# Kernel optimization log

Measured on AMD Instinct MI355X. Metric: run time of the kernel, lower is better.

Reference implementation:

```python
import jax, jax.numpy as jnp
import numpy as np
from jax import lax

B, S, D = 16, 1024, 1024
PE = 20          # positioning_embedding (LSTM hidden)
NB = 3           # num_building_blocks
EPS = 1e-12      # F.normalize eps


def setup_inputs() -> dict:
    key = jax.random.key(0)
    ks = jax.random.split(key, 10)
    s = lambda *sh: 0.05
    inp = {
        "x": jax.random.normal(ks[0], (B, S, D), dtype=jnp.float32),
        # LSTM params (PyTorch layout: gates ordered i,f,g,o)
        "W_ih": jax.random.normal(ks[1], (4 * PE, D), dtype=jnp.float32) * 0.02,
        "W_hh": jax.random.normal(ks[2], (4 * PE, PE), dtype=jnp.float32) * 0.02,
        "b_ih": jax.random.normal(ks[3], (4 * PE,), dtype=jnp.float32) * 0.02,
        "b_hh": jax.random.normal(ks[4], (4 * PE,), dtype=jnp.float32) * 0.02,
        # mu_generator: Linear(PE -> NB)
        "W_mu": jax.random.normal(ks[5], (NB, PE), dtype=jnp.float32) * 0.1,
        "b_mu": jax.random.normal(ks[6], (NB,), dtype=jnp.float32) * 0.1,
        # sigma_generator: Linear(PE -> 1)
        "W_sig": jax.random.normal(ks[7], (1, PE), dtype=jnp.float32) * 0.1,
        "b_sig": jax.random.normal(ks[8], (1,), dtype=jnp.float32) * 0.1,
    }
    return inp


def _lstm(x, W_ih, W_hh, b_ih, b_hh):
    # x: [B, S, D] -> h: [B, S, PE]; single-layer batch_first LSTM, h0=c0=0
    b, _, _ = x.shape
    H = W_hh.shape[1]
    xg = jnp.einsum("bsd,gd->bsg", x, W_ih) + b_ih + b_hh  # [B,S,4H]

    def step(carry, xg_t):
        h, c = carry
        g = xg_t + h @ W_hh.T
        i, f, gg, o = jnp.split(g, 4, axis=-1)
        c = jax.nn.sigmoid(f) * c + jax.nn.sigmoid(i) * jnp.tanh(gg)
        h = jax.nn.sigmoid(o) * jnp.tanh(c)
        return (h, c), h

    init = (jnp.zeros((b, H), x.dtype), jnp.zeros((b, H), x.dtype))
    _, hs = lax.scan(step, init, xg.transpose(1, 0, 2))  # hs: [S,B,H]
    return hs.transpose(1, 0, 2)


def _forward(x, W_ih, W_hh, b_ih, b_hh, W_mu, b_mu, W_sig, b_sig):
    b, s, d = x.shape
    pw = _lstm(x, W_ih, W_hh, b_ih, b_hh)                       # [B,S,PE]
    mu_w = jax.nn.relu(jnp.einsum("bsp,np->bsn", pw, W_mu) + b_mu)   # [B,S,3]
    sigma = jax.nn.sigmoid(jnp.einsum("bsp,op->bso", pw, W_sig) + b_sig)[..., 0]  # [B,S]

    # sequential mu recurrence: mu_j = w0*prev_mu + w1*(1/S) + w2*(j+1)/S
    j_idx = jnp.arange(s, dtype=x.dtype)

    def mu_step(prev_mu, inputs):
        w_t, j = inputs  # w_t: [B,3]
        mu = w_t[:, 0] * prev_mu + w_t[:, 1] / s + w_t[:, 2] * (j + 1.0) / s
        return mu, mu

    _, mus = lax.scan(mu_step, jnp.zeros((b,), x.dtype),
                      (mu_w.transpose(1, 0, 2), j_idx))          # mus: [S,B]
    mu = mus.T                                                    # [B,S]

    # triangular relative positions: rel[j,i] = i/(j+1) for i<=j
    i_idx = jnp.arange(s, dtype=x.dtype)
    rel = i_idx[None, :] / (j_idx[:, None] + 1.0)                 # [S,S]
    mask = i_idx[None, :] <= j_idx[:, None]                       # lower-triangular

    w = jnp.exp(-((rel[None] - mu[:, :, None]) ** 2)
                / (2.0 * sigma[:, :, None] ** 2))                 # [B,S,S]
    w = jnp.where(mask[None], w, 0.0)
    # F.normalize over the position axis (L2)
    norm = jnp.sqrt(jnp.sum(w * w, axis=-1, keepdims=True))
    w = w / jnp.maximum(norm, EPS)

    context = jnp.einsum("bji,bid->bjd", w, x)                    # [B,S,D]
    return context


def reference(x, W_ih, W_hh, b_ih, b_hh, W_mu, b_mu, W_sig, b_sig):
    return _forward(x, W_ih, W_hh, b_ih, b_hh, W_mu, b_mu, W_sig, b_sig)
```

## Files before the change

### kernel.cpp

```cpp
#include <hip/hip_runtime.h>

#define DEVFN __device__ __forceinline__

static constexpr int cB  = 16;
static constexpr int cS  = 1024;
static constexpr int cD  = 1024;
static constexpr int cPE = 20;
static constexpr int cG  = 80;

typedef float  floatx2  __attribute__((ext_vector_type(2)));
typedef float  floatx4  __attribute__((ext_vector_type(4)));
typedef float  floatx16 __attribute__((ext_vector_type(16)));
typedef short  short8   __attribute__((ext_vector_type(8)));
typedef unsigned uintx2 __attribute__((ext_vector_type(2)));

DEVFN unsigned pack_bf(float a, float b) {
  union { float f; unsigned u; } ua, ub; ua.f = a; ub.f = b;
  return (ua.u >> 16) | (ub.u & 0xffff0000u);
}

static constexpr int K1_XS = 68;

__global__ __launch_bounds__(256) void k1_xg(
    const float* __restrict__ x, const float* __restrict__ W_ih,
    const float* __restrict__ b_ih, const float* __restrict__ b_hh,
    float* __restrict__ xgT, unsigned short* __restrict__ xbf_t, int use_bf)
{
  __shared__ float xs[64 * K1_XS];
  __shared__ float wsm[80 * K1_XS];

  const int t  = threadIdx.x;
  const int rg = t >> 4, cg = t & 15;
  const int r0 = rg * 4, c0 = cg * 5;
  const int row0 = blockIdx.x * 64;
  const int b  = row0 >> 10;
  const int s0 = row0 & 1023;

  floatx2 acc[4][5];
#pragma unroll
  for (int q = 0; q < 4; ++q)
#pragma unroll
    for (int cc = 0; cc < 5; ++cc) { acc[q][cc].x = 0.f; acc[q][cc].y = 0.f; }

  for (int kc = 0; kc < 16; ++kc) {
    const int k0 = kc * 64;
    {
      const int sr = t >> 2, sc = t & 3;
      const float4* src = (const float4*)(x + (size_t)(row0 + sr) * cD + k0 + sc * 16);
      float4 v0 = src[0], v1 = src[1], v2 = src[2], v3 = src[3];
      float4* dst = (float4*)&xs[sr * K1_XS + sc * 16];
      dst[0] = v0; dst[1] = v1; dst[2] = v2; dst[3] = v3;
    }
#pragma unroll
    for (int q = 0; q < 5; ++q) {
      const int id = t + q * 256;
      const int g = id >> 4, c4 = id & 15;
      float4 wv = *(const float4*)(W_ih + (size_t)g * cD + k0 + c4 * 4);
      *(float4*)&wsm[g * K1_XS + c4 * 4] = wv;
    }
    __syncthreads();

    if (use_bf) {
      const int dl = t >> 2, sc4 = t & 3;
      float v[16];
#pragma unroll
      for (int e = 0; e < 16; ++e) v[e] = xs[(sc4 * 16 + e) * K1_XS + dl];
      unsigned u[8];
#pragma unroll
      for (int p = 0; p < 8; ++p) u[p] = pack_bf(v[2 * p], v[2 * p + 1]);
      unsigned short* dstp = xbf_t + ((size_t)(b * cD + k0 + dl)) * cS + s0 + sc4 * 16;
      *(uint4*)dstp       = make_uint4(u[0], u[1], u[2], u[3]);
      *(uint4*)(dstp + 8) = make_uint4(u[4], u[5], u[6], u[7]);
    }

#pragma unroll 4
    for (int k2 = 0; k2 < 32; ++k2) {
      floatx2 xv[4], wv[5];
#pragma unroll
      for (int q = 0; q < 4; ++q)
        xv[q] = *(const floatx2*)&xs[(r0 + q) * K1_XS + 2 * k2];
#pragma unroll
      for (int cc = 0; cc < 5; ++cc)
        wv[cc] = *(const floatx2*)&wsm[(c0 + cc) * K1_XS + 2 * k2];
#pragma unroll
      for (int q = 0; q < 4; ++q)
#pragma unroll
        for (int cc = 0; cc < 5; ++cc)
          acc[q][cc] += xv[q] * wv[cc];
    }
    __syncthreads();
  }

#pragma unroll
  for (int cc = 0; cc < 5; ++cc) {
    const int g = c0 + cc;
    const float sc = (g >= 40 && g < 60) ? 2.88539008f : 1.44269504f;
    const float bs = b_ih[g] + b_hh[g];
    float4 v;
    v.x = (acc[0][cc].x + acc[0][cc].y + bs) * sc;
    v.y = (acc[1][cc].x + acc[1][cc].y + bs) * sc;
    v.z = (acc[2][cc].x + acc[2][cc].y + bs) * sc;
    v.w = (acc[3][cc].x + acc[3][cc].y + bs) * sc;
    *(float4*)&xgT[((size_t)(b * cG + g)) * cS + s0 + r0] = v;
  }
}

__global__ __launch_bounds__(64) void k2_lstm(
    const float* __restrict__ xgT, const float* __restrict__ W_hh,
    float* __restrict__ hbuf)
{
  const int b    = blockIdx.x;
  const int lane = threadIdx.x;
  const int half = lane >> 5;
  const int l31  = lane & 31;
  const int j    = (l31 < cPE) ? l31 : (cPE - 1);
  const float LOG2E = 1.44269504f, TWOLOG2E = 2.88539008f;

  const int rowA = half ? (20 + j) : j;
  const int rowB = half ? (60 + j) : (40 + j);
  const float sB   = half ? LOG2E : TWOLOG2E;
  const float subB = half ? 0.f : 1.f;

  floatx2 wA[10], wB[10];
#pragma unroll
  for (int p = 0; p < 10; ++p) {
    wA[p].x = W_hh[rowA * cPE + 2 * p]     * LOG2E;
    wA[p].y = W_hh[rowA * cPE + 2 * p + 1] * LOG2E;
    wB[p].x = W_hh[rowB * cPE + 2 * p]     * sB;
    wB[p].y = W_hh[rowB * cPE + 2 * p + 1] * sB;
  }

  const float* baseA = xgT + ((size_t)(b * cG + rowA)) * cS;
  const float* baseB = xgT + ((size_t)(b * cG + rowB)) * cS;

  float4 bufA[4], bufB[4];
#pragma unroll
  for (int s = 0; s < 4; ++s) {
    bufA[s] = *(const float4*)(baseA + s * 4);
    bufB[s] = *(const float4*)(baseB + s * 4);
  }

  unsigned long long hp[10];
#pragma unroll
  for (int p = 0; p < 10; ++p) hp[p] = 0ull;

  float c = 0.f;
  float* hb = hbuf + (size_t)b * cS * cPE + j;

  for (int q0 = 0; q0 < 256; q0 += 4) {
#pragma unroll
    for (int s = 0; s < 4; ++s) {
      const int q = q0 + s;
      const float4 gA4 = bufA[s];
      const float4 gB4 = bufB[s];
      bufA[s] = *(const float4*)(baseA + (q + 4) * 4);
      bufB[s] = *(const float4*)(baseB + (q + 4) * 4);
#pragma unroll
      for (int e = 0; e < 4; ++e) {
        const float geA = (e == 0) ? gA4.x : (e == 1) ? gA4.y : (e == 2) ? gA4.z : gA4.w;
        const float geB = (e == 0) ? gB4.x : (e == 1) ? gB4.y : (e == 2) ? gB4.z : gB4.w;

        floatx2 aA0, aA1, aB0, aB1;
        aA0.x = geA; aA0.y = 0.f; aA1.x = 0.f; aA1.y = 0.f;
        aB0.x = geB; aB0.y = 0.f; aB1.x = 0.f; aB1.y = 0.f;
#pragma unroll
        for (int p = 0; p < 5; ++p) {
          asm("v_pk_fma_f32 %0, %1, %2, %0" : "+v"(aA0) : "v"(wA[p]),     "s"(hp[p]));
          asm("v_pk_fma_f32 %0, %1, %2, %0" : "+v"(aA1) : "v"(wA[5 + p]), "s"(hp[5 + p]));
          asm("v_pk_fma_f32 %0, %1, %2, %0" : "+v"(aB0) : "v"(wB[p]),     "s"(hp[p]));
          asm("v_pk_fma_f32 %0, %1, %2, %0" : "+v"(aB1) : "v"(wB[5 + p]), "s"(hp[5 + p]));
        }
        const float gAv = (aA0.x + aA0.y) + (aA1.x + aA1.y);
        const float gBv = (aB0.x + aB0.y) + (aB1.x + aB1.y);

        const float eA   = __builtin_amdgcn_exp2f(fminf(gAv, 30.f));
        const float actA = eA * __builtin_amdgcn_rcpf(eA + 1.f);
        const float eB   = __builtin_amdgcn_exp2f(fminf(gBv, 30.f));
        const float actB = (eB - subB) * __builtin_amdgcn_rcpf(eB + 1.f);

        union { float f; unsigned u; } ca, cb;
        ca.f = actA; cb.f = actB;
        uintx2 rA = __builtin_amdgcn_permlane32_swap(ca.u, ca.u, false, false);
        uintx2 rB = __builtin_amdgcn_permlane32_swap(cb.u, cb.u, false, false);
        union { unsigned u; float f; } vf, vi, vg, vo;
        vi.u = rA.x; vf.u = rA.y; vg.u = rB.x; vo.u = rB.y;

        c = vf.f * c + vi.f * vg.f;
        const float ec = __builtin_amdgcn_exp2f(fminf(TWOLOG2E * c, 30.f));
        const float th = (ec - 1.f) * __builtin_amdgcn_rcpf(ec + 1.f);
        const float hj = vo.f * th;

        if (lane < cPE) hb[(size_t)(q * 4 + e) * cPE] = hj;

        union { float f; unsigned u; } ch; ch.f = hj;
        const int hbits = (int)ch.u;
        const unsigned l0  = (unsigned)__builtin_amdgcn_readlane(hbits, 0);
        const unsigned l1  = (unsigned)__builtin_amdgcn_readlane(hbits, 1);
        const unsigned l2  = (unsigned)__builtin_amdgcn_readlane(hbits, 2);
        const unsigned l3  = (unsigned)__builtin_amdgcn_readlane(hbits, 3);
        const unsigned l4  = (unsigned)__builtin_amdgcn_readlane(hbits, 4);
        const unsigned l5  = (unsigned)__builtin_amdgcn_readlane(hbits, 5);
        const unsigned l6  = (unsigned)__builtin_amdgcn_readlane(hbits, 6);
        const unsigned l7  = (unsigned)__builtin_amdgcn_readlane(hbits, 7);
        const unsigned l8  = (unsigned)__builtin_amdgcn_readlane(hbits, 8);
        const unsigned l9  = (unsigned)__builtin_amdgcn_readlane(hbits, 9);
        const unsigned l10 = (unsigned)__builtin_amdgcn_readlane(hbits, 10);
        const unsigned l11 = (unsigned)__builtin_amdgcn_readlane(hbits, 11);
        const unsigned l12 = (unsigned)__builtin_amdgcn_readlane(hbits, 12);
        const unsigned l13 = (unsigned)__builtin_amdgcn_readlane(hbits, 13);
        const unsigned l14 = (unsigned)__builtin_amdgcn_readlane(hbits, 14);
        const unsigned l15 = (unsigned)__builtin_amdgcn_readlane(hbits, 15);
        const unsigned l16 = (unsigned)__builtin_amdgcn_readlane(hbits, 16);
        const unsigned l17 = (unsigned)__builtin_amdgcn_readlane(hbits, 17);
        const unsigned l18 = (unsigned)__builtin_amdgcn_readlane(hbits, 18);
        const unsigned l19 = (unsigned)__builtin_amdgcn_readlane(hbits, 19);
        hp[0] = (unsigned long long)l0  | ((unsigned long long)l1  << 32);
        hp[1] = (unsigned long long)l2  | ((unsigned long long)l3  << 32);
        hp[2] = (unsigned long long)l4  | ((unsigned long long)l5  << 32);
        hp[3] = (unsigned long long)l6  | ((unsigned long long)l7  << 32);
        hp[4] = (unsigned long long)l8  | ((unsigned long long)l9  << 32);
        hp[5] = (unsigned long long)l10 | ((unsigned long long)l11 << 32);
        hp[6] = (unsigned long long)l12 | ((unsigned long long)l13 << 32);
        hp[7] = (unsigned long long)l14 | ((unsigned long long)l15 << 32);
        hp[8] = (unsigned long long)l16 | ((unsigned long long)l17 << 32);
        hp[9] = (unsigned long long)l18 | ((unsigned long long)l19 << 32);
      }
    }
  }
}

__global__ __launch_bounds__(256) void k3a_muw(
    const float* __restrict__ hbuf,
    const float* __restrict__ W_mu, const float* __restrict__ b_mu,
    const float* __restrict__ W_sig, const float* __restrict__ b_sig,
    float* __restrict__ muwT, float* __restrict__ sigma)
{
  __shared__ float sw[84];
  const int t = threadIdx.x;
  if (t < 60) sw[t] = W_mu[t];
  else if (t < 80) sw[t] = W_sig[t - 60];
  else if (t < 83) sw[t] = b_mu[t - 80];
  else if (t == 83) sw[t] = b_sig[0];
  __syncthreads();

  const int r = blockIdx.x * 256 + t;
  const float4* hp = (const float4*)(hbuf + (size_t)r * cPE);
  float h[20];
#pragma unroll
  for (int q2 = 0; q2 < 5; ++q2) {
    float4 v = hp[q2];
    h[4 * q2] = v.x; h[4 * q2 + 1] = v.y; h[4 * q2 + 2] = v.z; h[4 * q2 + 3] = v.w;
  }
  float m0 = sw[80], m1 = sw[81], m2 = sw[82], sg = sw[83];
#pragma unroll
  for (int p = 0; p < 20; ++p) {
    m0 += sw[p]      * h[p];
    m1 += sw[20 + p] * h[p];
    m2 += sw[40 + p] * h[p];
    sg += sw[60 + p] * h[p];
  }
  muwT[r]                 = fmaxf(m0, 0.f);
  muwT[cB * cS + r]       = fmaxf(m1, 0.f);
  muwT[2 * cB * cS + r]   = fmaxf(m2, 0.f);
  sigma[r] = __builtin_amdgcn_rcpf(1.f + __builtin_amdgcn_exp2f(-1.44269504f * sg));
}

__global__ __launch_bounds__(64) void k3b_mu(
    const float* __restrict__ muwT, float* __restrict__ mu)
{
  const int t = threadIdx.x;
  if (t >= cB) return;
  const float* s0p = muwT + (size_t)t * cS;
  const float* s1p = muwT + cB * cS + (size_t)t * cS;
  const float* s2p = muwT + 2 * cB * cS + (size_t)t * cS;
  float* mb = mu + (size_t)t * cS;
  const float inv = 1.f / (float)cS;

  float4 a0 = *(const float4*)(s0p);
  float4 a1 = *(const float4*)(s1p);
  float4 a2 = *(const float4*)(s2p);
  float4 n0 = *(const float4*)(s0p + 4);
  float4 n1 = *(const float4*)(s1p + 4);
  float4 n2 = *(const float4*)(s2p + 4);

  float m = 0.f;
  for (int t4 = 0; t4 < 256; ++t4) {
    float4 w0 = a0, w1 = a1, w2 = a2;
    a0 = n0; a1 = n1; a2 = n2;
    if (t4 < 254) {
      n0 = *(const float4*)(s0p + t4 * 4 + 8);
      n1 = *(const float4*)(s1p + t4 * 4 + 8);
      n2 = *(const float4*)(s2p + t4 * 4 + 8);
    }
    const int tt = t4 * 4;
    m = w0.x * m + (w1.x + w2.x * (float)(tt + 1)) * inv; mb[tt]     = m;
    m = w0.y * m + (w1.y + w2.y * (float)(tt + 2)) * inv; mb[tt + 1] = m;
    m = w0.z * m + (w1.z + w2.z * (float)(tt + 3)) * inv; mb[tt + 2] = m;
    m = w0.w * m + (w1.w + w2.w * (float)(tt + 4)) * inv; mb[tt + 3] = m;
  }
}

static constexpr int TJ = 64, TD = 128, KI = 32, RS = 40;

__global__ __launch_bounds__(256) void k4_attn(
    const float* __restrict__ x, const unsigned short* __restrict__ xbf_t,
    int use_bf, const float* __restrict__ mu, const float* __restrict__ sigma,
    float* __restrict__ out)
{
  __shared__ unsigned short xsT[TD * RS];
  __shared__ float snrm[2][32];
  __shared__ float sscl[2][32];

  const int b   = blockIdx.z;
  const int jt0 = blockIdx.x * TJ;
  const int dt0 = blockIdx.y * TD;
  const int tid = threadIdx.x;
  const int wave = tid >> 6, lane = tid & 63;
  const int jh = wave & 1, dh = wave >> 1;
  const int n32 = lane & 31, half = lane >> 5;
  const int jrow = jt0 + jh * 32 + n32;

  const float muv  = mu[b * cS + jrow];
  const float sg   = sigma[b * cS + jrow];
  const float invj = 1.f / (float)(jrow + 1);
  const float ce   = -0.72134752f / (sg * sg);

  float nrm2 = 0.f;
  floatx16 acc0 = (floatx16)0.f, acc1 = (floatx16)0.f;

  const int iend = jt0 + TJ;
  for (int i0 = 0; i0 < iend; i0 += KI) {
    __syncthreads();
    if (use_bf) {
#pragma unroll
      for (int q = 0; q < 2; ++q) {
        const int cc = tid + q * 256;
        const int dl = cc >> 2, part = cc & 3;
        uint4 v = *(const uint4*)(xbf_t + ((size_t)(b * cD + dt0 + dl)) * cS + i0 + part * 8);
        *(uint4*)&xsT[dl * RS + part * 8] = v;
      }
    } else {
#pragma unroll
      for (int q = 0; q < 2; ++q) {
        const int cc = tid + q * 256;
        const int i = cc & 31, d8 = cc >> 5;
        const float* xp = x + ((size_t)(b * cS + i0 + i)) * cD + dt0 + d8 * 8;
        float4 f0 = *(const float4*)xp;
        float4 f1 = *(const float4*)(xp + 4);
        float vv[8] = {f0.x, f0.y, f0.z, f0.w, f1.x, f1.y, f1.z, f1.w};
#pragma unroll
        for (int e = 0; e < 8; ++e) {
          union { float f; unsigned u; } cv; cv.f = vv[e];
          xsT[(d8 * 8 + e) * RS + i] = (unsigned short)(cv.u >> 16);
        }
      }
    }
    __syncthreads();

    short8 af0, af1;
#pragma unroll
    for (int kc = 0; kc < 2; ++kc) {
      short8 af;
#pragma unroll
      for (int e = 0; e < 8; ++e) {
        const int ig = i0 + kc * 16 + half * 8 + e;
        const float d = fmaf((float)ig, invj, -muv);
        float w = __builtin_amdgcn_exp2f(ce * d * d);
        w = (ig <= jrow) ? w : 0.f;
        nrm2 += w * w;
        union { float f; unsigned u; } cv; cv.f = w;
        af[e] = (short)(cv.u >> 16);
      }
      if (kc == 0) af0 = af; else af1 = af;
    }

    const int rbase = dh * 64 + n32;
    short8 b00 = *(const short8*)&xsT[(rbase)      * RS + half * 8];
    short8 b01 = *(const short8*)&xsT[(rbase)      * RS + 16 + half * 8];
    short8 b10 = *(const short8*)&xsT[(rbase + 32) * RS + half * 8];
    short8 b11 = *(const short8*)&xsT[(rbase + 32) * RS + 16 + half * 8];
    acc0 = __builtin_amdgcn_mfma_f32_32x32x16_bf16(af0, b00, acc0, 0, 0, 0);
    acc0 = __builtin_amdgcn_mfma_f32_32x32x16_bf16(af1, b01, acc0, 0, 0, 0);
    acc1 = __builtin_amdgcn_mfma_f32_32x32x16_bf16(af0, b10, acc1, 0, 0, 0);
    acc1 = __builtin_amdgcn_mfma_f32_32x32x16_bf16(af1, b11, acc1, 0, 0, 0);
  }

  nrm2 += __shfl_xor(nrm2, 32);
  if (wave < 2 && half == 0) snrm[jh][n32] = nrm2;
  __syncthreads();
  if (tid < 64)
    sscl[tid >> 5][tid & 31] =
        __builtin_amdgcn_rcpf(fmaxf(sqrtf(snrm[tid >> 5][tid & 31]), 1e-12f));
  __syncthreads();

  float srow[16];
#pragma unroll
  for (int reg = 0; reg < 16; ++reg) {
    const int row = (reg & 3) + 8 * (reg >> 2) + 4 * half;
    srow[reg] = sscl[jh][row];
  }
#pragma unroll
  for (int reg = 0; reg < 16; ++reg) {
    const int row = (reg & 3) + 8 * (reg >> 2) + 4 * half;
    const int jg = jt0 + jh * 32 + row;
    const int d0 = dt0 + dh * 64 + n32;
    out[((size_t)(b * cS + jg)) * cD + d0]      = acc0[reg] * srow[reg];
    out[((size_t)(b * cS + jg)) * cD + d0 + 32] = acc1[reg] * srow[reg];
  }
}

extern "C" void kernel_launch(void* const* d_in, const int* in_sizes, int n_in,
                              void* d_out, int out_size, void* d_ws, size_t ws_size,
                              hipStream_t stream) {
  const float* x     = (const float*)d_in[0];
  const float* W_ih  = (const float*)d_in[1];
  const float* W_hh  = (const float*)d_in[2];
  const float* b_ih  = (const float*)d_in[3];
  const float* b_hh  = (const float*)d_in[4];
  const float* W_mu  = (const float*)d_in[5];
  const float* b_mu  = (const float*)d_in[6];
  const float* W_sig = (const float*)d_in[7];
  const float* b_sig = (const float*)d_in[8];
  float* out = (float*)d_out;

  char* ws = (char*)d_ws;
  const size_t off_xg  = 0;
  const size_t off_h   = off_xg  + (size_t)cB*cS*cG*4;
  const size_t off_muw = off_h   + (size_t)cB*cS*cPE*4;
  const size_t off_sig = off_muw + (size_t)cB*cS*3*4;
  const size_t off_mu  = off_sig + (size_t)cB*cS*4;
  const size_t off_xbf = off_mu  + (size_t)cB*cS*4;
  const size_t need_bf = off_xbf + (size_t)cB*cS*cD*2;

  float* xgT   = (float*)(ws + off_xg);
  float* hbuf  = (float*)(ws + off_h);
  float* muwT  = (float*)(ws + off_muw);
  float* sigma = (float*)(ws + off_sig);
  float* mu    = (float*)(ws + off_mu);
  unsigned short* xbf_t = (unsigned short*)(ws + off_xbf);
  const int use_bf = (ws_size >= need_bf) ? 1 : 0;

  k1_xg  <<<dim3(cB * cS / 64), dim3(256), 0, stream>>>(x, W_ih, b_ih, b_hh, xgT, xbf_t, use_bf);
  k2_lstm<<<dim3(cB),           dim3(64),  0, stream>>>(xgT, W_hh, hbuf);
  k3a_muw<<<dim3(cB * cS / 256), dim3(256), 0, stream>>>(hbuf, W_mu, b_mu, W_sig, b_sig, muwT, sigma);
  k3b_mu <<<dim3(1),            dim3(64),  0, stream>>>(muwT, mu);
  k4_attn<<<dim3(cS/TJ, cD/TD, cB), dim3(256), 0, stream>>>(x, xbf_t, use_bf, mu, sigma, out);
}
```

Before: 496.9 us.

## Double-buffer attention LDS tiles and deepen mu-scan prefetch

The attention kernel now uses two LDS buffers, so the next x tile is staged while the current tile's weights and MFMAs are computed, leaving one barrier per iteration instead of two. The serial mu recurrence kernel now prefetches eight float4 groups ahead instead of two, to hide global load latency in the single-thread-per-batch scan. The cost is doubled LDS use in the attention kernel, which may reduce occupancy, and more registers in the mu kernel.

```diff
diff --git a/kernel.cpp b/kernel.cpp
--- a/kernel.cpp
+++ b/kernel.cpp
@@ -276,27 +276,31 @@
   float* mb = mu + (size_t)t * cS;
   const float inv = 1.f / (float)cS;
 
-  float4 a0 = *(const float4*)(s0p);
-  float4 a1 = *(const float4*)(s1p);
-  float4 a2 = *(const float4*)(s2p);
-  float4 n0 = *(const float4*)(s0p + 4);
-  float4 n1 = *(const float4*)(s1p + 4);
-  float4 n2 = *(const float4*)(s2p + 4);
+  float4 b0[8], b1[8], b2[8];
+#pragma unroll
+  for (int u = 0; u < 8; ++u) {
+    b0[u] = *(const float4*)(s0p + u * 4);
+    b1[u] = *(const float4*)(s1p + u * 4);
+    b2[u] = *(const float4*)(s2p + u * 4);
+  }
 
   float m = 0.f;
-  for (int t4 = 0; t4 < 256; ++t4) {
-    float4 w0 = a0, w1 = a1, w2 = a2;
-    a0 = n0; a1 = n1; a2 = n2;
-    if (t4 < 254) {
-      n0 = *(const float4*)(s0p + t4 * 4 + 8);
-      n1 = *(const float4*)(s1p + t4 * 4 + 8);
-      n2 = *(const float4*)(s2p + t4 * 4 + 8);
-    }
-    const int tt = t4 * 4;
-    m = w0.x * m + (w1.x + w2.x * (float)(tt + 1)) * inv; mb[tt]     = m;
-    m = w0.y * m + (w1.y + w2.y * (float)(tt + 2)) * inv; mb[tt + 1] = m;
-    m = w0.z * m + (w1.z + w2.z * (float)(tt + 3)) * inv; mb[tt + 2] = m;
-    m = w0.w * m + (w1.w + w2.w * (float)(tt + 4)) * inv; mb[tt + 3] = m;
+  for (int t8 = 0; t8 < 32; ++t8) {
+#pragma unroll
+    for (int u = 0; u < 8; ++u) {
+      const int t4 = t8 * 8 + u;
+      float4 w0 = b0[u], w1 = b1[u], w2 = b2[u];
+      if (t4 < 248) {
+        b0[u] = *(const float4*)(s0p + (t4 + 8) * 4);
+        b1[u] = *(const float4*)(s1p + (t4 + 8) * 4);
+        b2[u] = *(const float4*)(s2p + (t4 + 8) * 4);
+      }
+      const int tt = t4 * 4;
+      m = w0.x * m + (w1.x + w2.x * (float)(tt + 1)) * inv; mb[tt]     = m;
+      m = w0.y * m + (w1.y + w2.y * (float)(tt + 2)) * inv; mb[tt + 1] = m;
+      m = w0.z * m + (w1.z + w2.z * (float)(tt + 3)) * inv; mb[tt + 2] = m;
+      m = w0.w * m + (w1.w + w2.w * (float)(tt + 4)) * inv; mb[tt + 3] = m;
+    }
   }
 }
 
@@ -307,7 +311,7 @@
     int use_bf, const float* __restrict__ mu, const float* __restrict__ sigma,
     float* __restrict__ out)
 {
-  __shared__ unsigned short xsT[TD * RS];
+  __shared__ unsigned short xsT[2][TD * RS];
   __shared__ float snrm[2][32];
   __shared__ float sscl[2][32];
 
@@ -329,15 +333,15 @@
   floatx16 acc0 = (floatx16)0.f, acc1 = (floatx16)0.f;
 
   const int iend = jt0 + TJ;
-  for (int i0 = 0; i0 < iend; i0 += KI) {
-    __syncthreads();
+
+  auto stage = [&](int pb, int i0) {
     if (use_bf) {
 #pragma unroll
       for (int q = 0; q < 2; ++q) {
         const int cc = tid + q * 256;
         const int dl = cc >> 2, part = cc & 3;
         uint4 v = *(const uint4*)(xbf_t + ((size_t)(b * cD + dt0 + dl)) * cS + i0 + part * 8);
-        *(uint4*)&xsT[dl * RS + part * 8] = v;
+        *(uint4*)&xsT[pb][dl * RS + part * 8] = v;
       }
     } else {
 #pragma unroll
@@ -351,11 +355,18 @@
 #pragma unroll
         for (int e = 0; e < 8; ++e) {
           union { float f; unsigned u; } cv; cv.f = vv[e];
-          xsT[(d8 * 8 + e) * RS + i] = (unsigned short)(cv.u >> 16);
+          xsT[pb][(d8 * 8 + e) * RS + i] = (unsigned short)(cv.u >> 16);
         }
       }
     }
-    __syncthreads();
+  };
+
+  stage(0, 0);
+  __syncthreads();
+
+  int pb = 0;
+  for (int i0 = 0; i0 < iend; i0 += KI) {
+    if (i0 + KI < iend) stage(pb ^ 1, i0 + KI);
 
     short8 af0, af1;
 #pragma unroll
@@ -375,14 +386,17 @@
     }
 
     const int rbase = dh * 64 + n32;
-    short8 b00 = *(const short8*)&xsT[(rbase)      * RS + half * 8];
-    short8 b01 = *(const short8*)&xsT[(rbase)      * RS + 16 + half * 8];
-    short8 b10 = *(const short8*)&xsT[(rbase + 32) * RS + half * 8];
-    short8 b11 = *(const short8*)&xsT[(rbase + 32) * RS + 16 + half * 8];
+    short8 b00 = *(const short8*)&xsT[pb][(rbase)      * RS + half * 8];
+    short8 b01 = *(const short8*)&xsT[pb][(rbase)      * RS + 16 + half * 8];
+    short8 b10 = *(const short8*)&xsT[pb][(rbase + 32) * RS + half * 8];
+    short8 b11 = *(const short8*)&xsT[pb][(rbase + 32) * RS + 16 + half * 8];
     acc0 = __builtin_amdgcn_mfma_f32_32x32x16_bf16(af0, b00, acc0, 0, 0, 0);
     acc0 = __builtin_amdgcn_mfma_f32_32x32x16_bf16(af1, b01, acc0, 0, 0, 0);
     acc1 = __builtin_amdgcn_mfma_f32_32x32x16_bf16(af0, b10, acc1, 0, 0, 0);
     acc1 = __builtin_amdgcn_mfma_f32_32x32x16_bf16(af1, b11, acc1, 0, 0, 0);
+
+    __syncthreads();
+    pb ^= 1;
   }
 
   nrm2 += __shfl_xor(nrm2, 32);
```

Result: faster. 471.0 us (-5.2%).
